# Optimization experiments

Hardware: AMD Instinct MI355X
Metric: run time of the kernel (lower is better)

## Reference

```python
import jax, jax.numpy as jnp
import numpy as np

GAMMA = 0.5  # triplet_loss_gamma
B, N, M = 16, 2048, 2048


def setup_inputs() -> dict:
    key = jax.random.key(0)
    k1, k2, k3 = jax.random.split(key, 3)
    scores = jax.random.normal(k1, (B, N + 1, M + 1), dtype=jnp.float32)
    gt_matches0 = jax.random.randint(k2, (B, N), 0, M + 1, dtype=jnp.int32)
    gt_matches1 = jax.random.randint(k3, (B, M), 0, N + 1, dtype=jnp.int32)
    return {"scores": scores, "gt_matches0": gt_matches0, "gt_matches1": gt_matches1}


def reference(scores, gt_matches0, gt_matches1):
    b, n = gt_matches0.shape
    m = gt_matches1.shape[1]
    # -1 means unmatched -> dustbin index (m for rows, n for cols)
    gt0 = jnp.where(gt_matches0 == -1, m, gt_matches0)  # (b, n), values in [0, m]
    gt1 = jnp.where(gt_matches1 == -1, n, gt_matches1)  # (b, m), values in [0, n]

    # ---- anchor = rows (points in cloud 0) ----
    s_rows = scores[:, :n, :]                                  # (b, n, m+1)
    pos0 = jnp.take_along_axis(s_rows, gt0[:, :, None].astype(jnp.int32), axis=2)  # (b, n, 1)
    # negatives: all m columns except the positive one, in order (== boolean-mask gather)
    jidx = jnp.arange(m, dtype=jnp.int32)[None, None, :]       # (1, 1, m)
    neg_j = jidx + (jidx >= gt0[:, :, None]).astype(jnp.int32)  # skip positive column
    neg0 = jnp.take_along_axis(s_rows, neg_j, axis=2)          # (b, n, m)
    # -log(exp(pos)) - (-log(exp(neg))) == neg - pos
    before_clamp1 = neg0 - pos0                                # (b, n, m)
    gap1 = jnp.maximum(before_clamp1 + GAMMA, 0.0)
    loss_mean1 = jnp.mean(jnp.log(jnp.sum(gap1, axis=2) + 1.0), axis=1)  # (b,)

    # ---- anchor = columns (points in cloud 1) ----
    s_cols = scores[:, :, :m]                                  # (b, n+1, m)
    pos1 = jnp.take_along_axis(s_cols, gt1[:, None, :].astype(jnp.int32), axis=1)  # (b, 1, m)
    iidx = jnp.arange(n, dtype=jnp.int32)[None, :, None]       # (1, n, 1)
    neg_i = iidx + (iidx >= gt1[:, None, :]).astype(jnp.int32)  # skip positive row
    neg1 = jnp.take_along_axis(s_cols, neg_i, axis=1)          # (b, n, m)
    before_clamp2 = neg1 - pos1                                # (b, n, m)
    gap2 = jnp.maximum(before_clamp2 + GAMMA, 0.0)
    loss_mean2 = jnp.mean(jnp.log(jnp.sum(gap2, axis=1) + 1.0), axis=1)  # (b,)

    # variance regularizer over all margins (torch.var default: unbiased, ddof=1)
    margin = jnp.concatenate([before_clamp1, before_clamp2], axis=0)  # (2b, n, m)
    var_loss = jnp.log(jnp.var(margin, ddof=1) + 1.0)
    return (loss_mean1 + loss_mean2) / 2.0 + var_loss
```

## Files before the change

kernel.cpp:

```cpp
#include <hip/hip_runtime.h>
#include <math.h>

#define GAMMA 0.5f

constexpr int B_ = 16;
constexpr int N_ = 2048;
constexpr int M_ = 2048;
constexpr int S_ = 2049;
constexpr long long PLANE = (long long)S_ * S_;

constexpr int Q_      = 8;
constexpr int TILE_W  = 512;
constexpr int NTILE   = 4;
constexpr int RPW     = 16;
constexpr int RPB     = 64;
constexpr int NSTRIPE = (S_ + RPB - 1) / RPB;

constexpr int NDBL = 28;

__global__ void gather_pos(const float* __restrict__ scores,
                           const int* __restrict__ gt0,
                           const int* __restrict__ gt1,
                           float* __restrict__ pos0,
                           float* __restrict__ pos1,
                           double* __restrict__ D) {
  int idx = blockIdx.x * blockDim.x + threadIdx.x;
  if (idx < NDBL) D[idx] = 0.0;
  const int total = B_ * N_;
  if (idx < total) {
    int b = idx >> 11;
    int i = idx & (N_ - 1);
    int g = gt0[idx];
    if (g == -1) g = M_;
    pos0[idx] = scores[(long long)b * PLANE + (long long)i * S_ + g];
  } else if (idx < 2 * total) {
    int k = idx - total;
    int b = k >> 11;
    int j = k & (M_ - 1);
    int g = gt1[k];
    if (g == -1) g = N_;
    pos1[k] = scores[(long long)b * PLANE + (long long)g * S_ + j];
  }
}

__launch_bounds__(256)
__global__ void margin_main(const float* __restrict__ scores,
                            const float* __restrict__ pos0,
                            const float* __restrict__ pos1,
                            float* __restrict__ rowPart,
                            float* __restrict__ colPart,
                            double* __restrict__ D) {
  const int tile = blockIdx.x;
  const int st   = blockIdx.y;
  const int b    = blockIdx.z;
  const int i0   = st * RPB;
  const int tid  = threadIdx.x;
  const int lane = tid & 63;
  const int w    = tid >> 6;
  const int j0   = tile * TILE_W;

  __shared__ float lp0[RPB];
  __shared__ float ldsC[4][TILE_W];
  __shared__ float ldsM[4][8];

  if (tid < RPB) {
    int i = i0 + tid;
    lp0[tid] = (i < N_) ? pos0[b * N_ + i] : 0.0f;
  }

  float p1[Q_], cC[Q_];
#pragma unroll
  for (int q = 0; q < Q_; ++q) {
    p1[q] = pos1[b * M_ + j0 + 64 * q + lane];
    cC[q] = 0.0f;
  }
  float gs = 0.f, gq = 0.f, gsr = 0.f, gqr = 0.f,
        gsc = 0.f, gqc = 0.f, x0 = 0.f, x1 = 0.f;

  __syncthreads();

  const int ib = i0 + w * RPW;
  int rmax = S_ - ib;
  rmax = rmax < 0 ? 0 : (rmax > RPW ? RPW : rmax);
  const float* rowp = scores + (long long)b * PLANE + (long long)ib * S_ + j0 + lane;
  const bool last_tile = (tile == NTILE - 1);

#pragma unroll 2
  for (int r = 0; r < rmax; ++r) {
    const int i = ib + r;
    const float p0 = lp0[w * RPW + r];
    const bool lastrow = (i == N_);

    float s[Q_];
#pragma unroll
    for (int q = 0; q < Q_; ++q) s[q] = rowp[q * 64];
    float extra = 0.0f;
    if (last_tile && lane == 0) extra = rowp[TILE_W];

    float rC = 0.0f;
#pragma unroll
    for (int q = 0; q < Q_; ++q) {
      const float sv = s[q];
      const float sg = sv + GAMMA;
      rC += fmaxf(sg - p0, 0.0f);
      x0  = fmaf(p0, sv, x0);
      cC[q] += fmaxf(sg - p1[q], 0.0f);
      x1  = fmaf(p1[q], sv, x1);
      gs += sv;
      gq  = fmaf(sv, sv, gq);
      if (lastrow) { gsr += sv; gqr = fmaf(sv, sv, gqr); }
    }
    if (last_tile && lane == 0) {
      rC  += fmaxf(extra + GAMMA - p0, 0.0f);
      x0   = fmaf(p0, extra, x0);
      gs  += extra; gq  = fmaf(extra, extra, gq);
      gsc += extra; gqc = fmaf(extra, extra, gqc);
      if (lastrow) { gsr += extra; gqr = fmaf(extra, extra, gqr); }
    }

#pragma unroll
    for (int off = 32; off; off >>= 1) rC += __shfl_xor(rC, off, 64);
    if (lane == 0 && !lastrow)
      rowPart[((long long)tile * B_ + b) * N_ + i] = rC;
    rowp += S_;
  }

  float m0 = gs, m1 = gq, m2 = gsr, m3 = gqr, m4 = gsc, m5 = gqc, m6 = x0, m7 = x1;
#pragma unroll
  for (int off = 32; off; off >>= 1) {
    m0 += __shfl_xor(m0, off, 64); m1 += __shfl_xor(m1, off, 64);
    m2 += __shfl_xor(m2, off, 64); m3 += __shfl_xor(m3, off, 64);
    m4 += __shfl_xor(m4, off, 64); m5 += __shfl_xor(m5, off, 64);
    m6 += __shfl_xor(m6, off, 64); m7 += __shfl_xor(m7, off, 64);
  }
  if (lane == 0) {
    ldsM[w][0] = m0; ldsM[w][1] = m1; ldsM[w][2] = m2; ldsM[w][3] = m3;
    ldsM[w][4] = m4; ldsM[w][5] = m5; ldsM[w][6] = m6; ldsM[w][7] = m7;
  }
#pragma unroll
  for (int q = 0; q < Q_; ++q) ldsC[w][q * 64 + lane] = cC[q];

  __syncthreads();

  {
    const float c0v = ldsC[0][tid] + ldsC[1][tid] + ldsC[2][tid] + ldsC[3][tid];
    const float c1v = ldsC[0][tid + 256] + ldsC[1][tid + 256] +
                      ldsC[2][tid + 256] + ldsC[3][tid + 256];
    const long long base = ((long long)st * B_ + b) * M_ + j0;
    colPart[base + tid] = c0v;
    colPart[base + tid + 256] = c1v;
  }
  if (tid < 8) {
    double v = (double)ldsM[0][tid] + (double)ldsM[1][tid] +
               (double)ldsM[2][tid] + (double)ldsM[3][tid];
    atomicAdd(&D[tid], v);
  }
}

__global__ void finalize1(const float* __restrict__ rowPart,
                          const float* __restrict__ colPart,
                          const float* __restrict__ pos0,
                          const float* __restrict__ pos1,
                          double* __restrict__ D) {
  const int slice = blockIdx.x;
  const int b     = blockIdx.y;
  const int phase = blockIdx.z;
  const int tid   = threadIdx.x;
  const int lane  = tid & 63;
  const int w     = tid >> 6;
  const int idx   = slice * 256 + tid;

  double aL, aP, aPq;
  if (phase == 0) {
    float r = 0.f;
#pragma unroll
    for (int t = 0; t < NTILE; ++t)
      r += rowPart[((long long)t * B_ + b) * N_ + idx];
    float p = pos0[b * N_ + idx];
    aL = log((double)r + 0.5);
    aP = (double)p; aPq = (double)p * p;
  } else {
    float c = 0.f;
    for (int st = 0; st < NSTRIPE; ++st)
      c += colPart[((long long)st * B_ + b) * M_ + idx];
    float p = pos1[b * M_ + idx];
    aL = log((double)c + 0.5);
    aP = (double)p; aPq = (double)p * p;
  }

#pragma unroll
  for (int off = 32; off; off >>= 1) {
    aL  += __shfl_xor(aL, off, 64);
    aP  += __shfl_xor(aP, off, 64);
    aPq += __shfl_xor(aPq, off, 64);
  }
  __shared__ double red[4][3];
  if (lane == 0) { red[w][0] = aL; red[w][1] = aP; red[w][2] = aPq; }
  __syncthreads();
  if (tid == 0) {
    atomicAdd(&D[8 + b], red[0][0] + red[1][0] + red[2][0] + red[3][0]);
    atomicAdd(&D[24 + 2 * phase], red[0][1] + red[1][1] + red[2][1] + red[3][1]);
    atomicAdd(&D[25 + 2 * phase], red[0][2] + red[1][2] + red[2][2] + red[3][2]);
  }
}

__global__ void finalize2(const double* __restrict__ D,
                          float* __restrict__ out) {
  const int lane = threadIdx.x;
  const double G1 = D[0], G2 = D[1], G1r = D[2], G2r = D[3];
  const double G1c = D[4], G2c = D[5], X0 = D[6], X1 = D[7];
  const double P0 = D[24], P0q = D[25], P1 = D[26], P1q = D[27];
  const double SM = 2.0 * G1 - G1r - G1c - 2049.0 * (P0 + P1);
  const double SQ = 2.0 * G2 - G2r - G2c - 2.0 * (X0 + X1)
                    + 2049.0 * (P0q + P1q);
  const double cnt = 134217728.0;
  const double var = (SQ - SM * SM / cnt) / (cnt - 1.0);
  const double vl  = log(var + 1.0);
  if (lane < B_) out[lane] = (float)(D[8 + lane] / 4096.0 + vl);
}

extern "C" void kernel_launch(void* const* d_in, const int* in_sizes, int n_in,
                              void* d_out, int out_size, void* d_ws, size_t ws_size,
                              hipStream_t stream) {
  const float* scores = (const float*)d_in[0];
  const int*   gt0    = (const int*)d_in[1];
  const int*   gt1    = (const int*)d_in[2];
  float*       out    = (float*)d_out;

  double* D    = (double*)d_ws;
  float* pos0  = (float*)((char*)d_ws + 256);
  float* pos1  = pos0 + (size_t)B_ * N_;
  float* rowPart = pos1 + (size_t)B_ * M_;
  float* colPart = rowPart + (size_t)NTILE * B_ * N_;

  const int gth = 2 * B_ * N_;
  gather_pos<<<(gth + 255) / 256, 256, 0, stream>>>(scores, gt0, gt1,
                                                    pos0, pos1, D);

  dim3 grid(NTILE, NSTRIPE, B_);
  margin_main<<<grid, 256, 0, stream>>>(scores, pos0, pos1,
                                        rowPart, colPart, D);

  dim3 fgrid(8, B_, 2);
  finalize1<<<fgrid, 256, 0, stream>>>(rowPart, colPart, pos0, pos1, D);
  finalize2<<<1, 64, 0, stream>>>(D, out);
}
```

Baseline: 79.66 us.

## Software-pipeline row loads, hoist column sums, fuse finalize kernels

The main loop is double-buffered: the next row is loaded with nontemporal loads while the current one is computed. Per-element work is cut by precomputing gamma-minus-pos constants and accumulating per-column sums, so the pos1·s cross term and the global sum are formed once per column after the loop instead of per element. The two finalize kernels are merged using a last-block atomic counter, which removes one launch. In exchange the kernel uses more registers and LDS, and the last-block pattern relies on correct memory fences.

```diff
diff --git a/kernel.cpp b/kernel.cpp
--- a/kernel.cpp
+++ b/kernel.cpp
@@ -14,9 +14,9 @@
 constexpr int NTILE   = 4;
 constexpr int RPW     = 16;
 constexpr int RPB     = 64;
-constexpr int NSTRIPE = (S_ + RPB - 1) / RPB;
-
-constexpr int NDBL = 28;
+constexpr int NSTRIPE = 33;
+
+constexpr int NDBL = 32;
 
 __global__ void gather_pos(const float* __restrict__ scores,
                            const int* __restrict__ gt0,
@@ -54,114 +54,155 @@
   const int st   = blockIdx.y;
   const int b    = blockIdx.z;
   const int i0   = st * RPB;
+  const int j0   = tile * TILE_W;
   const int tid  = threadIdx.x;
   const int lane = tid & 63;
   const int w    = tid >> 6;
-  const int j0   = tile * TILE_W;
-
-  __shared__ float lp0[RPB];
-  __shared__ float ldsC[4][TILE_W];
-  __shared__ float ldsM[4][8];
+
+  __shared__ float  lp0[RPB];
+  __shared__ float  ldsC[4][TILE_W];
+  __shared__ float  ldsS[4][TILE_W];
+  __shared__ float  ldsM[4][6];
+  __shared__ double ldsF[4][2];
 
   if (tid < RPB) {
     int i = i0 + tid;
     lp0[tid] = (i < N_) ? pos0[b * N_ + i] : 0.0f;
   }
 
-  float p1[Q_], cC[Q_];
+  float c1[Q_], cC[Q_], cS[Q_];
 #pragma unroll
   for (int q = 0; q < Q_; ++q) {
-    p1[q] = pos1[b * M_ + j0 + 64 * q + lane];
-    cC[q] = 0.0f;
-  }
-  float gs = 0.f, gq = 0.f, gsr = 0.f, gqr = 0.f,
-        gsc = 0.f, gqc = 0.f, x0 = 0.f, x1 = 0.f;
+    c1[q] = GAMMA - pos1[b * M_ + j0 + 64 * q + lane];
+    cC[q] = 0.f; cS[q] = 0.f;
+  }
+  float x0 = 0.f, gqA = 0.f, gqB = 0.f, gsr = 0.f, gqr = 0.f,
+        gsc = 0.f, gqc = 0.f;
 
   __syncthreads();
 
   const int ib = i0 + w * RPW;
   int rmax = S_ - ib;
   rmax = rmax < 0 ? 0 : (rmax > RPW ? RPW : rmax);
-  const float* rowp = scores + (long long)b * PLANE + (long long)ib * S_ + j0 + lane;
-  const bool last_tile = (tile == NTILE - 1);
-
-#pragma unroll 2
-  for (int r = 0; r < rmax; ++r) {
+  const float* rp = scores + (long long)b * PLANE + (long long)ib * S_ + j0 + lane;
+  const bool exlane = (tile == NTILE - 1) && (lane == 0);
+
+  float sA[Q_], sB[Q_], eA = 0.f, eB = 0.f;
+
+  auto LOADROW = [&](float (&s)[Q_], float& e, const float* p) {
+#pragma unroll
+    for (int q = 0; q < Q_; ++q) s[q] = __builtin_nontemporal_load(p + q * 64);
+    if (exlane) e = __builtin_nontemporal_load(p + TILE_W);
+  };
+
+  auto COMPUTE = [&](const float (&s)[Q_], float e, int r) {
     const int i = ib + r;
     const float p0 = lp0[w * RPW + r];
-    const bool lastrow = (i == N_);
-
-    float s[Q_];
-#pragma unroll
-    for (int q = 0; q < Q_; ++q) s[q] = rowp[q * 64];
-    float extra = 0.0f;
-    if (last_tile && lane == 0) extra = rowp[TILE_W];
-
-    float rC = 0.0f;
+    const float c0 = GAMMA - p0;
+    float rc0 = 0.f, rc1 = 0.f, rs0 = 0.f, rs1 = 0.f;
 #pragma unroll
     for (int q = 0; q < Q_; ++q) {
       const float sv = s[q];
-      const float sg = sv + GAMMA;
-      rC += fmaxf(sg - p0, 0.0f);
-      x0  = fmaf(p0, sv, x0);
-      cC[q] += fmaxf(sg - p1[q], 0.0f);
-      x1  = fmaf(p1[q], sv, x1);
-      gs += sv;
-      gq  = fmaf(sv, sv, gq);
-      if (lastrow) { gsr += sv; gqr = fmaf(sv, sv, gqr); }
+      float t0 = fmaxf(sv + c0, 0.f);
+      float t1 = fmaxf(sv + c1[q], 0.f);
+      if (q & 1) { rc1 += t0; rs1 += sv; gqB = fmaf(sv, sv, gqB); }
+      else       { rc0 += t0; rs0 += sv; gqA = fmaf(sv, sv, gqA); }
+      cC[q] += t1;
+      cS[q] += sv;
     }
-    if (last_tile && lane == 0) {
-      rC  += fmaxf(extra + GAMMA - p0, 0.0f);
-      x0   = fmaf(p0, extra, x0);
-      gs  += extra; gq  = fmaf(extra, extra, gq);
-      gsc += extra; gqc = fmaf(extra, extra, gqc);
-      if (lastrow) { gsr += extra; gqr = fmaf(extra, extra, gqr); }
+    float rC   = rc0 + rc1;
+    float rsum = rs0 + rs1;
+    if (exlane) {
+      rC   += fmaxf(e + c0, 0.f);
+      rsum += e;
+      gqA   = fmaf(e, e, gqA);
+      gsc  += e;
+      gqc   = fmaf(e, e, gqc);
     }
-
+    x0 = fmaf(p0, rsum, x0);
+    if (i == N_) {
+      gsr += rsum;
+#pragma unroll
+      for (int q = 0; q < Q_; ++q) gqr = fmaf(s[q], s[q], gqr);
+      if (exlane) gqr = fmaf(e, e, gqr);
+    }
 #pragma unroll
     for (int off = 32; off; off >>= 1) rC += __shfl_xor(rC, off, 64);
-    if (lane == 0 && !lastrow)
+    if (lane == 0 && i < N_)
       rowPart[((long long)tile * B_ + b) * N_ + i] = rC;
-    rowp += S_;
-  }
-
-  float m0 = gs, m1 = gq, m2 = gsr, m3 = gqr, m4 = gsc, m5 = gqc, m6 = x0, m7 = x1;
+  };
+
+  if (rmax > 0) {
+    LOADROW(sA, eA, rp);
+    int r = 0;
+    for (; r + 2 <= rmax; r += 2) {
+      LOADROW(sB, eB, rp + S_);
+      COMPUTE(sA, eA, r);
+      const float* pn = (r + 2 < rmax) ? rp + 2 * S_ : rp;
+      LOADROW(sA, eA, pn);
+      COMPUTE(sB, eB, r + 1);
+      rp += 2 * S_;
+    }
+    if (r < rmax) COMPUTE(sA, eA, r);
+  }
+
+  float m0 = gqA + gqB, m1 = gsr, m2 = gqr, m3 = gsc, m4 = gqc, m5 = x0;
 #pragma unroll
   for (int off = 32; off; off >>= 1) {
     m0 += __shfl_xor(m0, off, 64); m1 += __shfl_xor(m1, off, 64);
     m2 += __shfl_xor(m2, off, 64); m3 += __shfl_xor(m3, off, 64);
     m4 += __shfl_xor(m4, off, 64); m5 += __shfl_xor(m5, off, 64);
-    m6 += __shfl_xor(m6, off, 64); m7 += __shfl_xor(m7, off, 64);
   }
   if (lane == 0) {
-    ldsM[w][0] = m0; ldsM[w][1] = m1; ldsM[w][2] = m2; ldsM[w][3] = m3;
-    ldsM[w][4] = m4; ldsM[w][5] = m5; ldsM[w][6] = m6; ldsM[w][7] = m7;
-  }
-#pragma unroll
-  for (int q = 0; q < Q_; ++q) ldsC[w][q * 64 + lane] = cC[q];
-
-  __syncthreads();
-
-  {
-    const float c0v = ldsC[0][tid] + ldsC[1][tid] + ldsC[2][tid] + ldsC[3][tid];
-    const float c1v = ldsC[0][tid + 256] + ldsC[1][tid + 256] +
-                      ldsC[2][tid + 256] + ldsC[3][tid + 256];
-    const long long base = ((long long)st * B_ + b) * M_ + j0;
-    colPart[base + tid] = c0v;
-    colPart[base + tid + 256] = c1v;
-  }
-  if (tid < 8) {
+    ldsM[w][0] = m0; ldsM[w][1] = m1; ldsM[w][2] = m2;
+    ldsM[w][3] = m3; ldsM[w][4] = m4; ldsM[w][5] = m5;
+  }
+#pragma unroll
+  for (int q = 0; q < Q_; ++q) {
+    ldsC[w][q * 64 + lane] = cC[q];
+    ldsS[w][q * 64 + lane] = cS[q];
+  }
+  __syncthreads();
+
+  const float cc0 = ldsC[0][tid] + ldsC[1][tid] + ldsC[2][tid] + ldsC[3][tid];
+  const float cc1 = ldsC[0][tid + 256] + ldsC[1][tid + 256] +
+                    ldsC[2][tid + 256] + ldsC[3][tid + 256];
+  const float ss0 = ldsS[0][tid] + ldsS[1][tid] + ldsS[2][tid] + ldsS[3][tid];
+  const float ss1 = ldsS[0][tid + 256] + ldsS[1][tid + 256] +
+                    ldsS[2][tid + 256] + ldsS[3][tid + 256];
+  const long long cb = ((long long)st * B_ + b) * M_ + j0;
+  colPart[cb + tid]       = cc0;
+  colPart[cb + tid + 256] = cc1;
+
+  const float p1a = pos1[b * M_ + j0 + tid];
+  const float p1b = pos1[b * M_ + j0 + tid + 256];
+  float g1p = ss0 + ss1;
+  float x1p = p1a * ss0 + p1b * ss1;
+#pragma unroll
+  for (int off = 32; off; off >>= 1) {
+    g1p += __shfl_xor(g1p, off, 64);
+    x1p += __shfl_xor(x1p, off, 64);
+  }
+  if (lane == 0) { ldsF[w][0] = (double)g1p; ldsF[w][1] = (double)x1p; }
+  __syncthreads();
+
+  if (tid == 0) {
+    atomicAdd(&D[0], ldsF[0][0] + ldsF[1][0] + ldsF[2][0] + ldsF[3][0]);
+    atomicAdd(&D[7], ldsF[0][1] + ldsF[1][1] + ldsF[2][1] + ldsF[3][1]);
+  }
+  if (tid < 6) {
     double v = (double)ldsM[0][tid] + (double)ldsM[1][tid] +
                (double)ldsM[2][tid] + (double)ldsM[3][tid];
-    atomicAdd(&D[tid], v);
+    atomicAdd(&D[1 + tid], v);
   }
 }
 
-__global__ void finalize1(const float* __restrict__ rowPart,
-                          const float* __restrict__ colPart,
-                          const float* __restrict__ pos0,
-                          const float* __restrict__ pos1,
-                          double* __restrict__ D) {
+__global__ void finalize(const float* __restrict__ rowPart,
+                         const float* __restrict__ colPart,
+                         const float* __restrict__ pos0,
+                         const float* __restrict__ pos1,
+                         double* __restrict__ D,
+                         float* __restrict__ out) {
   const int slice = blockIdx.x;
   const int b     = blockIdx.y;
   const int phase = blockIdx.z;
@@ -181,8 +222,8 @@
     aP = (double)p; aPq = (double)p * p;
   } else {
     float c = 0.f;
-    for (int st = 0; st < NSTRIPE; ++st)
-      c += colPart[((long long)st * B_ + b) * M_ + idx];
+    for (int s = 0; s < NSTRIPE; ++s)
+      c += colPart[((long long)s * B_ + b) * M_ + idx];
     float p = pos1[b * M_ + idx];
     aL = log((double)c + 0.5);
     aP = (double)p; aPq = (double)p * p;
@@ -202,21 +243,34 @@
     atomicAdd(&D[24 + 2 * phase], red[0][1] + red[1][1] + red[2][1] + red[3][1]);
     atomicAdd(&D[25 + 2 * phase], red[0][2] + red[1][2] + red[2][2] + red[3][2]);
   }
-}
-
-__global__ void finalize2(const double* __restrict__ D,
-                          float* __restrict__ out) {
-  const int lane = threadIdx.x;
-  const double G1 = D[0], G2 = D[1], G1r = D[2], G2r = D[3];
-  const double G1c = D[4], G2c = D[5], X0 = D[6], X1 = D[7];
-  const double P0 = D[24], P0q = D[25], P1 = D[26], P1q = D[27];
-  const double SM = 2.0 * G1 - G1r - G1c - 2049.0 * (P0 + P1);
-  const double SQ = 2.0 * G2 - G2r - G2c - 2.0 * (X0 + X1)
-                    + 2049.0 * (P0q + P1q);
-  const double cnt = 134217728.0;
-  const double var = (SQ - SM * SM / cnt) / (cnt - 1.0);
-  const double vl  = log(var + 1.0);
-  if (lane < B_) out[lane] = (float)(D[8 + lane] / 4096.0 + vl);
+
+  __shared__ int lastFlag;
+  if (tid == 0) {
+    __threadfence();
+    int* cnt = (int*)(D + 28);
+    int old = __hip_atomic_fetch_add(cnt, 1, __ATOMIC_ACQ_REL,
+                                     __HIP_MEMORY_SCOPE_AGENT);
+    lastFlag = (old == 8 * B_ * 2 - 1);
+  }
+  __syncthreads();
+  if (lastFlag && tid == 0) {
+    double Dv[28];
+    for (int k = 0; k < 28; ++k)
+      Dv[k] = __hip_atomic_load(&D[k], __ATOMIC_RELAXED,
+                                __HIP_MEMORY_SCOPE_AGENT);
+    const double CS = Dv[0], G2 = Dv[1], G1r = Dv[2], G2r = Dv[3];
+    const double G1c = Dv[4], G2c = Dv[5], X0 = Dv[6], X1 = Dv[7];
+    const double P0 = Dv[24], P0q = Dv[25], P1 = Dv[26], P1q = Dv[27];
+    const double G1 = CS + G1c;
+    const double SM = 2.0 * G1 - G1r - G1c - 2049.0 * (P0 + P1);
+    const double SQ = 2.0 * G2 - G2r - G2c - 2.0 * (X0 + X1)
+                      + 2049.0 * (P0q + P1q);
+    const double cnt_ = 134217728.0;
+    const double var = (SQ - SM * SM / cnt_) / (cnt_ - 1.0);
+    const double vl = log(var + 1.0);
+    for (int k = 0; k < B_; ++k)
+      out[k] = (float)(Dv[8 + k] / 4096.0 + vl);
+  }
 }
 
 extern "C" void kernel_launch(void* const* d_in, const int* in_sizes, int n_in,
@@ -227,9 +281,9 @@
   const int*   gt1    = (const int*)d_in[2];
   float*       out    = (float*)d_out;
 
-  double* D    = (double*)d_ws;
-  float* pos0  = (float*)((char*)d_ws + 256);
-  float* pos1  = pos0 + (size_t)B_ * N_;
+  double* D      = (double*)d_ws;
+  float* pos0    = (float*)((char*)d_ws + 256);
+  float* pos1    = pos0 + (size_t)B_ * N_;
   float* rowPart = pos1 + (size_t)B_ * M_;
   float* colPart = rowPart + (size_t)NTILE * B_ * N_;
 
@@ -242,6 +296,5 @@
                                         rowPart, colPart, D);
 
   dim3 fgrid(8, B_, 2);
-  finalize1<<<fgrid, 256, 0, stream>>>(rowPart, colPart, pos0, pos1, D);
-  finalize2<<<1, 64, 0, stream>>>(D, out);
+  finalize<<<fgrid, 256, 0, stream>>>(rowPart, colPart, pos0, pos1, D, out);
 }
```

After: 130.6 us. 63.9% more time.
